# Optimization experiments

Measured on AMD Instinct MI355X. Metric: run time of the kernel, lower is better.

Reference implementation:

```python
import jax, jax.numpy as jnp
import numpy as np

B, S, H, HKV, D, BS = 2, 2048, 32, 8, 128, 16
HIDDEN = H * D            # 4096
G = H // HKV              # 4 query heads per kv head
NB = S // BS              # 128 blocks per sequence
SCALE = D ** -0.5


def setup_inputs() -> dict:
    key = jax.random.key(0)
    k1, k2, k3 = jax.random.split(key, 3)
    T = B * S
    hidden_states = jax.random.normal(k1, (T, HIDDEN), dtype=jnp.float32)
    w_qkv = jax.random.normal(k2, (HIDDEN, HIDDEN + 2 * HKV * D), dtype=jnp.float32) * 0.02
    w_out = jax.random.normal(k3, (HIDDEN, HIDDEN), dtype=jnp.float32) * 0.02
    k_cache = jnp.zeros((B * NB, HKV, BS, D), dtype=jnp.float32)
    v_cache = jnp.zeros((B * NB, HKV, BS, D), dtype=jnp.float32)
    block_tables = jnp.arange(B * NB, dtype=jnp.int32).reshape(B, NB)
    return {"hidden_states": hidden_states, "w_qkv": w_qkv, "w_out": w_out,
            "k_cache": k_cache, "v_cache": v_cache, "block_tables": block_tables}


def reference(hidden_states, w_qkv, w_out, k_cache, v_cache, block_tables):
    # qkv projection on packed tokens [T, hidden]
    qkv = hidden_states @ w_qkv
    q, k, v = jnp.split(qkv, [HIDDEN, HIDDEN + HKV * D], axis=-1)
    q = q.reshape(B, S, H, D)
    k = k.reshape(B, S, HKV, D)
    v = v.reshape(B, S, HKV, D)

    # --- paged KV store: scatter per-block pages into cache via block_tables ---
    # [B, NB, BS, HKV, D] -> page layout [B, NB, HKV, BS, D]
    k_pages = k.reshape(B, NB, BS, HKV, D).transpose(0, 1, 3, 2, 4)
    v_pages = v.reshape(B, NB, BS, HKV, D).transpose(0, 1, 3, 2, 4)
    k_cache = k_cache.at[block_tables].set(k_pages)
    v_cache = v_cache.at[block_tables].set(v_pages)

    # --- paged KV gather for prefill attention ---
    kg = k_cache[block_tables].transpose(0, 2, 1, 3, 4).reshape(B, HKV, S, D)
    vg = v_cache[block_tables].transpose(0, 2, 1, 3, 4).reshape(B, HKV, S, D)

    # GQA causal attention: group query heads per kv head
    qh = q.transpose(0, 2, 1, 3).reshape(B, HKV, G, S, D)
    scores = jnp.einsum('bhgqd,bhkd->bhgqk', qh, kg) * SCALE
    causal = jnp.tril(jnp.ones((S, S), dtype=bool))
    scores = jnp.where(causal, scores, -jnp.inf)
    attn = jax.nn.softmax(scores, axis=-1)
    out = jnp.einsum('bhgqk,bhkd->bhgqd', attn, vg)   # [B,HKV,G,S,D]
    out = out.reshape(B, H, S, D).transpose(0, 2, 1, 3).reshape(B * S, HIDDEN)
    return out @ w_out
```

## Files before the change

kernel.cpp:

```cpp
#include <hip/hip_runtime.h>

#define BB 2
#define SS 2048
#define HH 32
#define HKV 8
#define DD 128
#define HIDDEN 4096
#define NQK 6144
#define TT 4096
#define SCALE 0.08838834764831843f
#define SCALE_LOG2E 0.12751743444f

typedef __attribute__((ext_vector_type(8), __may_alias__)) short short8;
typedef __attribute__((ext_vector_type(4), __may_alias__)) short short4v;
typedef __attribute__((ext_vector_type(4), __may_alias__)) float floatx4;
typedef __attribute__((ext_vector_type(4), __may_alias__)) float f4;

__device__ __forceinline__ short f2bf(float x) {
    unsigned u = __builtin_bit_cast(unsigned, x);
    u += 0x7FFFu + ((u >> 16) & 1u);
    return (short)(u >> 16);
}

__device__ __forceinline__ void gload_lds16(const short* g, short* l) {
    __builtin_amdgcn_global_load_lds((const __attribute__((address_space(1))) void*)g,
                                     (__attribute__((address_space(3))) void*)l, 16, 0, 0);
}

__global__ __launch_bounds__(256) void cvt_f32_bf16(const float* __restrict__ src,
                                                    short* __restrict__ dst) {
    int i = blockIdx.x * 256 + threadIdx.x;
    f4 v = ((const f4*)src)[i];
    short4v o = { f2bf(v.x), f2bf(v.y), f2bf(v.z), f2bf(v.w) };
    ((short4v*)dst)[i] = o;
}

__global__ __launch_bounds__(256) void transpose_cvt(const float* __restrict__ src,
                                                     short* __restrict__ dst,
                                                     int rows, int cols) {
    __shared__ float t[64][65];
    int c0 = blockIdx.x * 64, r0 = blockIdx.y * 64;
    int tx = threadIdx.x & 15, ty = threadIdx.x >> 4;
#pragma unroll
    for (int i = 0; i < 64; i += 16) {
        f4 v = *(const f4*)(src + (size_t)(r0 + ty + i) * cols + c0 + tx * 4);
        t[ty + i][tx * 4 + 0] = v.x;
        t[ty + i][tx * 4 + 1] = v.y;
        t[ty + i][tx * 4 + 2] = v.z;
        t[ty + i][tx * 4 + 3] = v.w;
    }
    __syncthreads();
    int ox = threadIdx.x & 7, oy = threadIdx.x >> 3;
#pragma unroll
    for (int i = 0; i < 64; i += 32) {
        int cc = oy + i;
        short8 s;
#pragma unroll
        for (int j = 0; j < 8; j++) s[j] = f2bf(t[ox * 8 + j][cc]);
        *(short8*)(dst + (size_t)(c0 + cc) * rows + r0 + ox * 8) = s;
    }
}

__global__ __launch_bounds__(256) void build_vt(const short* __restrict__ qkv,
                                                short* __restrict__ vt) {
    __shared__ short t[32][33];
    int tx = threadIdx.x, ty = threadIdx.y;
    int s0 = blockIdx.x * 32, d0 = blockIdx.y * 32;
    int bh = blockIdx.z; int b = bh >> 3, hk = bh & 7;
#pragma unroll
    for (int i = 0; i < 32; i += 8)
        t[ty + i][tx] = qkv[(size_t)(b * SS + s0 + ty + i) * NQK + 5120 + hk * DD + d0 + tx];
    __syncthreads();
#pragma unroll
    for (int i = 0; i < 32; i += 8)
        vt[(size_t)(bh * DD + d0 + ty + i) * SS + s0 + tx] = t[tx][ty + i];
}

template <int OUT_BF16>
__global__ __launch_bounds__(512, 2) void gemm_bt(const short* __restrict__ A,
                                                  const short* __restrict__ Bt,
                                                  void* __restrict__ Cout,
                                                  int M, int N, int K) {
    (void)M;
    __shared__ __align__(16) short smem[65536];
    const int tid  = threadIdx.x;
    const int wave = tid >> 6, lane = tid & 63;
    const int qn = lane & 15, quad = lane >> 4;
    const int wm = wave >> 2, wn = wave & 3;

    int bid = blockIdx.y * gridDim.x + blockIdx.x;
    int xcd = bid & 7, idx = bid >> 3;
    int bnx = gridDim.x >> 2;
    int xm = xcd & 1, xn = xcd >> 1;
    int im = idx & 7, in_ = idx >> 3;
    const int m0 = (xm * 8 + im) * 256;
    const int n0 = (xn * bnx + in_) * 256;

    const int NT = K >> 6;

    const int srow = tid >> 3;
    const int scg  = (tid & 7) ^ (srow & 7);
    const short* aS = A  + (size_t)(m0 + srow) * K + scg * 8;
    const short* bS = Bt + (size_t)(n0 + srow) * K + scg * 8;
    const int lwo = wave * 512;

#define STAGE_A(buf, blk, tt) gload_lds16(aS + (size_t)(blk) * 64 * K + (size_t)(tt) * 64, \
                                          smem + (buf) + (blk) * 4096 + lwo)
#define STAGE_B(buf, blk, tt) gload_lds16(bS + (size_t)(blk) * 64 * K + (size_t)(tt) * 64, \
                                          smem + (buf) + 16384 + (blk) * 4096 + lwo)

    const int xorm  = (qn & 7) << 3;
    const int a_row = (wm * 128 + qn) * 64;
    const int b_row = (wn * 64 + qn) * 64;
    const int col0  = (quad * 8) ^ xorm;
    const int col1  = col0 ^ 32;

#pragma unroll
    for (int blk = 0; blk < 4; blk++) { STAGE_A(0, blk, 0); STAGE_B(0, blk, 0); }
    if (NT > 1) {
#pragma unroll
        for (int blk = 0; blk < 4; blk++) { STAGE_A(32768, blk, 1); STAGE_B(32768, blk, 1); }
        asm volatile("s_waitcnt vmcnt(8)" ::: "memory");
    } else {
        asm volatile("s_waitcnt vmcnt(0)" ::: "memory");
    }
    __builtin_amdgcn_s_barrier();

    floatx4 acc[8][4] = {};

#pragma unroll 2
    for (int t = 0; t < NT; ++t) {
        const int cb = (t & 1) << 15;
        const short* Ab = smem + cb;
        const short* Bb = smem + cb + 16384;
        short8 a[4][2], b0[2][2], b1[2][2], a2[4][2];

#pragma unroll
        for (int mt = 0; mt < 4; mt++) {
            a[mt][0] = *(const short8*)(Ab + a_row + mt * 1024 + col0);
            a[mt][1] = *(const short8*)(Ab + a_row + mt * 1024 + col1);
        }
#pragma unroll
        for (int nt = 0; nt < 2; nt++) {
            b0[nt][0] = *(const short8*)(Bb + b_row + nt * 1024 + col0);
            b0[nt][1] = *(const short8*)(Bb + b_row + nt * 1024 + col1);
        }
        asm volatile("s_waitcnt lgkmcnt(8)" ::: "memory");
        __builtin_amdgcn_s_barrier();
        asm volatile("s_waitcnt lgkmcnt(0)" ::: "memory");
        __builtin_amdgcn_s_setprio(1);
#pragma unroll
        for (int mt = 0; mt < 4; mt++)
#pragma unroll
            for (int nt = 0; nt < 2; nt++) {
                acc[mt][nt] = __builtin_amdgcn_mfma_f32_16x16x32_bf16(a[mt][0], b0[nt][0], acc[mt][nt], 0, 0, 0);
                acc[mt][nt] = __builtin_amdgcn_mfma_f32_16x16x32_bf16(a[mt][1], b0[nt][1], acc[mt][nt], 0, 0, 0);
            }
        __builtin_amdgcn_s_setprio(0);
        __builtin_amdgcn_s_barrier();

#pragma unroll
        for (int nt = 0; nt < 2; nt++) {
            b1[nt][0] = *(const short8*)(Bb + b_row + 2048 + nt * 1024 + col0);
            b1[nt][1] = *(const short8*)(Bb + b_row + 2048 + nt * 1024 + col1);
        }
        if (t + 2 < NT) { STAGE_A(cb, 0, t + 2); STAGE_A(cb, 2, t + 2); }
        __builtin_amdgcn_s_barrier();
        asm volatile("s_waitcnt lgkmcnt(0)" ::: "memory");
        __builtin_amdgcn_s_setprio(1);
#pragma unroll
        for (int mt = 0; mt < 4; mt++)
#pragma unroll
            for (int nt = 0; nt < 2; nt++) {
                acc[mt][2 + nt] = __builtin_amdgcn_mfma_f32_16x16x32_bf16(a[mt][0], b1[nt][0], acc[mt][2 + nt], 0, 0, 0);
                acc[mt][2 + nt] = __builtin_amdgcn_mfma_f32_16x16x32_bf16(a[mt][1], b1[nt][1], acc[mt][2 + nt], 0, 0, 0);
            }
        __builtin_amdgcn_s_setprio(0);
        __builtin_amdgcn_s_barrier();

#pragma unroll
        for (int mt = 0; mt < 4; mt++) {
            a2[mt][0] = *(const short8*)(Ab + 4096 + a_row + mt * 1024 + col0);
            a2[mt][1] = *(const short8*)(Ab + 4096 + a_row + mt * 1024 + col1);
        }
        if (t + 2 < NT) { STAGE_B(cb, 0, t + 2); STAGE_B(cb, 1, t + 2);
                          STAGE_B(cb, 2, t + 2); STAGE_B(cb, 3, t + 2); }
        __builtin_amdgcn_s_barrier();
        asm volatile("s_waitcnt lgkmcnt(0)" ::: "memory");
        __builtin_amdgcn_s_setprio(1);
#pragma unroll
        for (int mt = 0; mt < 4; mt++)
#pragma unroll
            for (int nt = 0; nt < 2; nt++) {
                acc[4 + mt][2 + nt] = __builtin_amdgcn_mfma_f32_16x16x32_bf16(a2[mt][0], b1[nt][0], acc[4 + mt][2 + nt], 0, 0, 0);
                acc[4 + mt][2 + nt] = __builtin_amdgcn_mfma_f32_16x16x32_bf16(a2[mt][1], b1[nt][1], acc[4 + mt][2 + nt], 0, 0, 0);
            }
        __builtin_amdgcn_s_setprio(0);
        __builtin_amdgcn_s_barrier();

        if (t + 2 < NT) { STAGE_A(cb, 1, t + 2); STAGE_A(cb, 3, t + 2); }
        __builtin_amdgcn_s_setprio(1);
#pragma unroll
        for (int mt = 0; mt < 4; mt++)
#pragma unroll
            for (int nt = 0; nt < 2; nt++) {
                acc[4 + mt][nt] = __builtin_amdgcn_mfma_f32_16x16x32_bf16(a2[mt][0], b0[nt][0], acc[4 + mt][nt], 0, 0, 0);
                acc[4 + mt][nt] = __builtin_amdgcn_mfma_f32_16x16x32_bf16(a2[mt][1], b0[nt][1], acc[4 + mt][nt], 0, 0, 0);
            }
        __builtin_amdgcn_s_setprio(0);
        if (t + 2 < NT) asm volatile("s_waitcnt vmcnt(8)" ::: "memory");
        else            asm volatile("s_waitcnt vmcnt(0)" ::: "memory");
        __builtin_amdgcn_s_barrier();
    }
#undef STAGE_A
#undef STAGE_B

    const int erow = m0 + wm * 128 + quad * 4;
    const int ecol = n0 + wn * 64 + qn;
#pragma unroll
    for (int mt = 0; mt < 8; mt++)
#pragma unroll
        for (int nt = 0; nt < 4; nt++)
#pragma unroll
            for (int r = 0; r < 4; r++) {
                size_t off = (size_t)(erow + mt * 16 + r) * N + ecol + nt * 16;
                if (OUT_BF16) ((short*)Cout)[off] = f2bf(acc[mt][nt][r]);
                else          ((float*)Cout)[off] = acc[mt][nt][r];
            }
}

__global__ __launch_bounds__(512, 4) void attn_kernel(const short* __restrict__ qkv,
                                                      const short* __restrict__ vt,
                                                      short* __restrict__ out) {
    __shared__ __align__(16) short Kb[2 * 32 * 128];
    __shared__ __align__(16) short Vb[2 * 128 * 32];
    __shared__ __align__(16) short Ps[8 * 16 * 40];
    int tid = threadIdx.x, wave = tid >> 6, lane = tid & 63;
    int qn = lane & 15, quad = lane >> 4;
    int bid = blockIdx.x;
    int qt = 63 - (bid >> 4);
    int b  = (bid >> 3) & 1;
    int hk = bid & 7;
    int qb = qt * 32;
    int qh = wave >> 2;
    int h  = hk * 4 + (wave & 3);
    int bh = b * 8 + hk;
    int rowq = qb + qh * 16 + qn;

    short8 qf[4];
    {
        const short* qrow = qkv + (size_t)(b * SS + rowq) * NQK + h * DD;
#pragma unroll
        for (int c = 0; c < 4; c++) qf[c] = *(const short8*)(qrow + c * 32 + quad * 8);
    }
    const short8 onesv = { 0x3F80, 0x3F80, 0x3F80, 0x3F80, 0x3F80, 0x3F80, 0x3F80, 0x3F80 };
    floatx4 oacc[8] = {};
    floatx4 lacc = {};
    const int ntiles = qt + 1;

    const int kRow = tid >> 4;
    const int kCgp = (tid & 15) ^ (kRow & 7);
    const int vRow = tid >> 2;
    const int vCgp = (tid & 3) ^ ((vRow >> 1) & 3);
    const short* kSrc = qkv + (size_t)(b * SS) * NQK + HIDDEN + hk * DD + kCgp * 8;
    const short* vSrc = vt + (size_t)(bh * DD) * SS + vCgp * 8;
    short* kDst = Kb + wave * 512;
    short* vDst = Vb + wave * 512;

#define STAGEKV(buf, kb) do {                                                   \
        gload_lds16(kSrc + (size_t)((kb) + kRow) * NQK, kDst + (buf) * 4096);   \
        gload_lds16(vSrc + (size_t)vRow * SS + (kb),    vDst + (buf) * 4096);   \
    } while (0)

    STAGEKV(0, 0);
    __syncthreads();

    short* pw = Ps + wave * (16 * 40);
    for (int it = 0; it < ntiles; ++it) {
        const int kb = it * 32;
        const int cur = it & 1;
        if (it + 1 < ntiles) STAGEKV(cur ^ 1, kb + 32);
        const short* Kc = Kb + cur * 4096;
        const short* Vc = Vb + cur * 4096;

        floatx4 sc[2] = {};
#pragma unroll
        for (int c = 0; c < 4; c++) {
            int cg = (((c * 4 + quad) ^ (qn & 7)) * 8);
            short8 k0 = *(const short8*)(Kc + qn * 128 + cg);
            short8 k1 = *(const short8*)(Kc + (16 + qn) * 128 + cg);
            sc[0] = __builtin_amdgcn_mfma_f32_16x16x32_bf16(k0, qf[c], sc[0], 0, 0, 0);
            sc[1] = __builtin_amdgcn_mfma_f32_16x16x32_bf16(k1, qf[c], sc[1], 0, 0, 0);
        }

        const bool needMask = (kb + 31 > qb + qh * 16);
#pragma unroll
        for (int kt = 0; kt < 2; kt++) {
            float e[4];
#pragma unroll
            for (int r = 0; r < 4; r++) {
                float v = exp2f(sc[kt][r] * SCALE_LOG2E);
                bool masked = needMask && (kb + kt * 16 + quad * 4 + r > rowq);
                e[r] = masked ? 0.f : v;
            }
            short4v pk = { f2bf(e[0]), f2bf(e[1]), f2bf(e[2]), f2bf(e[3]) };
            *(short4v*)(pw + qn * 40 + kt * 16 + quad * 4) = pk;
        }
        short8 pf = *(const short8*)(pw + qn * 40 + quad * 8);

        __builtin_amdgcn_s_setprio(1);
#pragma unroll
        for (int dt = 0; dt < 8; dt++) {
            int vg = ((quad ^ ((qn >> 1) & 3)) * 8);
            short8 vf = *(const short8*)(Vc + (dt * 16 + qn) * 32 + vg);
            oacc[dt] = __builtin_amdgcn_mfma_f32_16x16x32_bf16(vf, pf, oacc[dt], 0, 0, 0);
        }
        lacc = __builtin_amdgcn_mfma_f32_16x16x32_bf16(onesv, pf, lacc, 0, 0, 0);
        __builtin_amdgcn_s_setprio(0);
        __syncthreads();
    }
#undef STAGEKV

    float inv = 1.0f / lacc[0];
    short* orow = out + (size_t)(b * SS + rowq) * HIDDEN + h * DD;
#pragma unroll
    for (int dt = 0; dt < 8; dt++) {
        short4v ov = { f2bf(oacc[dt][0] * inv), f2bf(oacc[dt][1] * inv),
                       f2bf(oacc[dt][2] * inv), f2bf(oacc[dt][3] * inv) };
        *(short4v*)(orow + dt * 16 + quad * 4) = ov;
    }
}

extern "C" void kernel_launch(void* const* d_in, const int* in_sizes, int n_in,
                              void* d_out, int out_size, void* d_ws, size_t ws_size,
                              hipStream_t stream) {
    (void)in_sizes; (void)n_in; (void)out_size; (void)ws_size;
    const float* hs    = (const float*)d_in[0];
    const float* w_qkv = (const float*)d_in[1];
    const float* w_out = (const float*)d_in[2];

    char* ws = (char*)d_ws;
    short* hsb   = (short*)(ws);
    short* wqkvT = (short*)(ws + 33554432);
    short* woutT = (short*)(ws + 83886080);
    short* qkv   = (short*)(ws + 117440512);
    short* vtb   = (short*)(ws + 167772160);
    short* attnb = (short*)(ws + 176160768);

    cvt_f32_bf16<<<16384, 256, 0, stream>>>(hs, hsb);
    transpose_cvt<<<dim3(NQK / 64, HIDDEN / 64), 256, 0, stream>>>(w_qkv, wqkvT, HIDDEN, NQK);
    transpose_cvt<<<dim3(HIDDEN / 64, HIDDEN / 64), 256, 0, stream>>>(w_out, woutT, HIDDEN, HIDDEN);
    gemm_bt<1><<<dim3(NQK / 256, TT / 256), 512, 0, stream>>>(hsb, wqkvT, qkv, TT, NQK, HIDDEN);
    build_vt<<<dim3(64, 4, 16), dim3(32, 8), 0, stream>>>(qkv, vtb);
    attn_kernel<<<1024, 512, 0, stream>>>(qkv, vtb, attnb);
    gemm_bt<0><<<dim3(HIDDEN / 256, TT / 256), 512, 0, stream>>>(attnb, woutT, d_out, TT, HIDDEN, HIDDEN);
}
```

Baseline: 712.3 us.

## Fuse prep conversion kernels and use 256x192 tiles for QKV GEMM

The three preprocessing kernels (hidden-state bf16 conversion and the two weight transpose-converts) are merged into one launch that dispatches on block index. The GEMM is templated on the number of N fragments per wave, and the QKV projection now uses 256x192 tiles. That gives 32x16=512 workgroups instead of 24x16=384 on the 256-CU part, for better wave-count balance. It also shrinks LDS per block and adjusts the vmcnt wait to match the fewer B loads, at the cost of lower arithmetic intensity per tile.

```diff
diff --git a/kernel.cpp b/kernel.cpp
--- a/kernel.cpp
+++ b/kernel.cpp
@@ -27,20 +27,29 @@
                                      (__attribute__((address_space(3))) void*)l, 16, 0, 0);
 }
 
-__global__ __launch_bounds__(256) void cvt_f32_bf16(const float* __restrict__ src,
-                                                    short* __restrict__ dst) {
-    int i = blockIdx.x * 256 + threadIdx.x;
-    f4 v = ((const f4*)src)[i];
-    short4v o = { f2bf(v.x), f2bf(v.y), f2bf(v.z), f2bf(v.w) };
-    ((short4v*)dst)[i] = o;
-}
-
-__global__ __launch_bounds__(256) void transpose_cvt(const float* __restrict__ src,
-                                                     short* __restrict__ dst,
-                                                     int rows, int cols) {
+__global__ __launch_bounds__(256) void prep_fused(const float* __restrict__ hs,
+                                                  short* __restrict__ hsb,
+                                                  const float* __restrict__ wq,
+                                                  short* __restrict__ wqT,
+                                                  const float* __restrict__ wo,
+                                                  short* __restrict__ woT) {
     __shared__ float t[64][65];
-    int c0 = blockIdx.x * 64, r0 = blockIdx.y * 64;
-    int tx = threadIdx.x & 15, ty = threadIdx.x >> 4;
+    int bid = blockIdx.x, tid = threadIdx.x;
+    if (bid < 16384) {
+        int i = bid * 256 + tid;
+        f4 v = ((const f4*)hs)[i];
+        short4v o = { f2bf(v.x), f2bf(v.y), f2bf(v.z), f2bf(v.w) };
+        ((short4v*)hsb)[i] = o;
+        return;
+    }
+    bid -= 16384;
+    const float* src; short* dst; int cols;
+    if (bid < 6144) { src = wq; dst = wqT; cols = NQK; }
+    else            { bid -= 6144; src = wo; dst = woT; cols = HIDDEN; }
+    const int rows = HIDDEN;
+    int ntx = cols >> 6;
+    int c0 = (bid % ntx) * 64, r0 = (bid / ntx) * 64;
+    int tx = tid & 15, ty = tid >> 4;
 #pragma unroll
     for (int i = 0; i < 64; i += 16) {
         f4 v = *(const f4*)(src + (size_t)(r0 + ty + i) * cols + c0 + tx * 4);
@@ -50,7 +59,7 @@
         t[ty + i][tx * 4 + 3] = v.w;
     }
     __syncthreads();
-    int ox = threadIdx.x & 7, oy = threadIdx.x >> 3;
+    int ox = tid & 7, oy = tid >> 3;
 #pragma unroll
     for (int i = 0; i < 64; i += 32) {
         int cc = oy + i;
@@ -76,13 +85,14 @@
         vt[(size_t)(bh * DD + d0 + ty + i) * SS + s0 + tx] = t[tx][ty + i];
 }
 
-template <int OUT_BF16>
+template <int OUT_BF16, int NFRAG>
 __global__ __launch_bounds__(512, 2) void gemm_bt(const short* __restrict__ A,
                                                   const short* __restrict__ Bt,
                                                   void* __restrict__ Cout,
                                                   int M, int N, int K) {
     (void)M;
-    __shared__ __align__(16) short smem[65536];
+    constexpr int BUFSZ = 16384 + NFRAG * 4096;
+    __shared__ __align__(16) short smem[2 * BUFSZ];
     const int tid  = threadIdx.x;
     const int wave = tid >> 6, lane = tid & 63;
     const int qn = lane & 15, quad = lane >> 4;
@@ -94,7 +104,7 @@
     int xm = xcd & 1, xn = xcd >> 1;
     int im = idx & 7, in_ = idx >> 3;
     const int m0 = (xm * 8 + im) * 256;
-    const int n0 = (xn * bnx + in_) * 256;
+    const int n0 = (xn * bnx + in_) * (NFRAG * 64);
 
     const int NT = K >> 6;
 
@@ -108,32 +118,38 @@
                                           smem + (buf) + (blk) * 4096 + lwo)
 #define STAGE_B(buf, blk, tt) gload_lds16(bS + (size_t)(blk) * 64 * K + (size_t)(tt) * 64, \
                                           smem + (buf) + 16384 + (blk) * 4096 + lwo)
+#define VMCNT_STEADY() do { if constexpr (NFRAG == 3) asm volatile("s_waitcnt vmcnt(7)" ::: "memory"); \
+                            else                      asm volatile("s_waitcnt vmcnt(8)" ::: "memory"); } while (0)
 
     const int xorm  = (qn & 7) << 3;
     const int a_row = (wm * 128 + qn) * 64;
-    const int b_row = (wn * 64 + qn) * 64;
+    const int b_row = (wn * (NFRAG * 16) + qn) * 64;
     const int col0  = (quad * 8) ^ xorm;
     const int col1  = col0 ^ 32;
 
 #pragma unroll
-    for (int blk = 0; blk < 4; blk++) { STAGE_A(0, blk, 0); STAGE_B(0, blk, 0); }
+    for (int blk = 0; blk < 4; blk++) STAGE_A(0, blk, 0);
+#pragma unroll
+    for (int blk = 0; blk < NFRAG; blk++) STAGE_B(0, blk, 0);
     if (NT > 1) {
 #pragma unroll
-        for (int blk = 0; blk < 4; blk++) { STAGE_A(32768, blk, 1); STAGE_B(32768, blk, 1); }
-        asm volatile("s_waitcnt vmcnt(8)" ::: "memory");
+        for (int blk = 0; blk < 4; blk++) STAGE_A(BUFSZ, blk, 1);
+#pragma unroll
+        for (int blk = 0; blk < NFRAG; blk++) STAGE_B(BUFSZ, blk, 1);
+        VMCNT_STEADY();
     } else {
         asm volatile("s_waitcnt vmcnt(0)" ::: "memory");
     }
     __builtin_amdgcn_s_barrier();
 
-    floatx4 acc[8][4] = {};
+    floatx4 acc[8][NFRAG] = {};
 
 #pragma unroll 2
     for (int t = 0; t < NT; ++t) {
-        const int cb = (t & 1) << 15;
+        const int cb = (t & 1) * BUFSZ;
         const short* Ab = smem + cb;
         const short* Bb = smem + cb + 16384;
-        short8 a[4][2], b0[2][2], b1[2][2], a2[4][2];
+        short8 a[4][2], b0[2][2], b1[NFRAG - 2][2], a2[4][2];
 
 #pragma unroll
         for (int mt = 0; mt < 4; mt++) {
@@ -160,9 +176,9 @@
         __builtin_amdgcn_s_barrier();
 
 #pragma unroll
-        for (int nt = 0; nt < 2; nt++) {
-            b1[nt][0] = *(const short8*)(Bb + b_row + 2048 + nt * 1024 + col0);
-            b1[nt][1] = *(const short8*)(Bb + b_row + 2048 + nt * 1024 + col1);
+        for (int nb = 0; nb < NFRAG - 2; nb++) {
+            b1[nb][0] = *(const short8*)(Bb + b_row + (2 + nb) * 1024 + col0);
+            b1[nb][1] = *(const short8*)(Bb + b_row + (2 + nb) * 1024 + col1);
         }
         if (t + 2 < NT) { STAGE_A(cb, 0, t + 2); STAGE_A(cb, 2, t + 2); }
         __builtin_amdgcn_s_barrier();
@@ -171,9 +187,9 @@
 #pragma unroll
         for (int mt = 0; mt < 4; mt++)
 #pragma unroll
-            for (int nt = 0; nt < 2; nt++) {
-                acc[mt][2 + nt] = __builtin_amdgcn_mfma_f32_16x16x32_bf16(a[mt][0], b1[nt][0], acc[mt][2 + nt], 0, 0, 0);
-                acc[mt][2 + nt] = __builtin_amdgcn_mfma_f32_16x16x32_bf16(a[mt][1], b1[nt][1], acc[mt][2 + nt], 0, 0, 0);
+            for (int nb = 0; nb < NFRAG - 2; nb++) {
+                acc[mt][2 + nb] = __builtin_amdgcn_mfma_f32_16x16x32_bf16(a[mt][0], b1[nb][0], acc[mt][2 + nb], 0, 0, 0);
+                acc[mt][2 + nb] = __builtin_amdgcn_mfma_f32_16x16x32_bf16(a[mt][1], b1[nb][1], acc[mt][2 + nb], 0, 0, 0);
             }
         __builtin_amdgcn_s_setprio(0);
         __builtin_amdgcn_s_barrier();
@@ -183,17 +199,19 @@
             a2[mt][0] = *(const short8*)(Ab + 4096 + a_row + mt * 1024 + col0);
             a2[mt][1] = *(const short8*)(Ab + 4096 + a_row + mt * 1024 + col1);
         }
-        if (t + 2 < NT) { STAGE_B(cb, 0, t + 2); STAGE_B(cb, 1, t + 2);
-                          STAGE_B(cb, 2, t + 2); STAGE_B(cb, 3, t + 2); }
+        if (t + 2 < NT) {
+#pragma unroll
+            for (int blk = 0; blk < NFRAG; blk++) STAGE_B(cb, blk, t + 2);
+        }
         __builtin_amdgcn_s_barrier();
         asm volatile("s_waitcnt lgkmcnt(0)" ::: "memory");
         __builtin_amdgcn_s_setprio(1);
 #pragma unroll
         for (int mt = 0; mt < 4; mt++)
 #pragma unroll
-            for (int nt = 0; nt < 2; nt++) {
-                acc[4 + mt][2 + nt] = __builtin_amdgcn_mfma_f32_16x16x32_bf16(a2[mt][0], b1[nt][0], acc[4 + mt][2 + nt], 0, 0, 0);
-                acc[4 + mt][2 + nt] = __builtin_amdgcn_mfma_f32_16x16x32_bf16(a2[mt][1], b1[nt][1], acc[4 + mt][2 + nt], 0, 0, 0);
+            for (int nb = 0; nb < NFRAG - 2; nb++) {
+                acc[4 + mt][2 + nb] = __builtin_amdgcn_mfma_f32_16x16x32_bf16(a2[mt][0], b1[nb][0], acc[4 + mt][2 + nb], 0, 0, 0);
+                acc[4 + mt][2 + nb] = __builtin_amdgcn_mfma_f32_16x16x32_bf16(a2[mt][1], b1[nb][1], acc[4 + mt][2 + nb], 0, 0, 0);
             }
         __builtin_amdgcn_s_setprio(0);
         __builtin_amdgcn_s_barrier();
@@ -208,19 +226,20 @@
                 acc[4 + mt][nt] = __builtin_amdgcn_mfma_f32_16x16x32_bf16(a2[mt][1], b0[nt][1], acc[4 + mt][nt], 0, 0, 0);
             }
         __builtin_amdgcn_s_setprio(0);
-        if (t + 2 < NT) asm volatile("s_waitcnt vmcnt(8)" ::: "memory");
+        if (t + 2 < NT) VMCNT_STEADY();
         else            asm volatile("s_waitcnt vmcnt(0)" ::: "memory");
         __builtin_amdgcn_s_barrier();
     }
 #undef STAGE_A
 #undef STAGE_B
+#undef VMCNT_STEADY
 
     const int erow = m0 + wm * 128 + quad * 4;
-    const int ecol = n0 + wn * 64 + qn;
+    const int ecol = n0 + wn * (NFRAG * 16) + qn;
 #pragma unroll
     for (int mt = 0; mt < 8; mt++)
 #pragma unroll
-        for (int nt = 0; nt < 4; nt++)
+        for (int nt = 0; nt < NFRAG; nt++)
 #pragma unroll
             for (int r = 0; r < 4; r++) {
                 size_t off = (size_t)(erow + mt * 16 + r) * N + ecol + nt * 16;
@@ -347,11 +366,9 @@
     short* vtb   = (short*)(ws + 167772160);
     short* attnb = (short*)(ws + 176160768);
 
-    cvt_f32_bf16<<<16384, 256, 0, stream>>>(hs, hsb);
-    transpose_cvt<<<dim3(NQK / 64, HIDDEN / 64), 256, 0, stream>>>(w_qkv, wqkvT, HIDDEN, NQK);
-    transpose_cvt<<<dim3(HIDDEN / 64, HIDDEN / 64), 256, 0, stream>>>(w_out, woutT, HIDDEN, HIDDEN);
-    gemm_bt<1><<<dim3(NQK / 256, TT / 256), 512, 0, stream>>>(hsb, wqkvT, qkv, TT, NQK, HIDDEN);
+    prep_fused<<<26624, 256, 0, stream>>>(hs, hsb, w_qkv, wqkvT, w_out, woutT);
+    gemm_bt<1, 3><<<dim3(NQK / 192, TT / 256), 512, 0, stream>>>(hsb, wqkvT, qkv, TT, NQK, HIDDEN);
     build_vt<<<dim3(64, 4, 16), dim3(32, 8), 0, stream>>>(qkv, vtb);
     attn_kernel<<<1024, 512, 0, stream>>>(qkv, vtb, attnb);
-    gemm_bt<0><<<dim3(HIDDEN / 256, TT / 256), 512, 0, stream>>>(attnb, woutT, d_out, TT, HIDDEN, HIDDEN);
-}
+    gemm_bt<0, 4><<<dim3(HIDDEN / 256, TT / 256), 512, 0, stream>>>(attnb, woutT, d_out, TT, HIDDEN, HIDDEN);
+}
```

After: 678.8 us. 1.05x faster.
